# Kernel optimization log

Measured on AMD Instinct MI355X. Metric: run time of the kernel, lower is better.

Reference implementation:

```python
import math
import jax, jax.numpy as jnp
import numpy as np


def setup_inputs() -> dict:
    key = jax.random.key(0)
    k1, k2, k3 = jax.random.split(key, 3)
    B, CK, CV = 2, 64, 384
    T, H, W = 8, 30, 54
    N = T * H * W
    mk = jax.random.normal(k1, (B, CK, N), dtype=jnp.float32)
    qk = jax.random.normal(k2, (B, CK, H, W), dtype=jnp.float32)
    mv = jax.random.normal(k3, (B, CV, N), dtype=jnp.float32)
    return {"mk": mk, "qk": qk, "mv": mv, "topk": 20}


def _compute_affinity(mk, qk, topk):
    # mk: [B, CK, N] memory keys; qk: [B, CK, H, W] query keys
    B, CK, H, W = qk.shape
    M = H * W
    qk2 = qk.reshape(B, CK, M)                      # [B, CK, M]
    a_sq = jnp.sum(mk * mk, axis=1)[:, :, None]     # [B, N, 1]
    ab = jnp.einsum('bcn,bcm->bnm', mk, qk2)        # [B, N, M]
    affinity = (2.0 * ab - a_sq) / math.sqrt(CK)    # negative sq-distance / sqrt(CK)
    N = affinity.shape[1]
    k = min(topk, N)
    # top-k over the memory axis (dim 1): move it last for lax.top_k
    aff_t = jnp.swapaxes(affinity, 1, 2)            # [B, M, N]
    vals, idx = jax.lax.top_k(aff_t, k)             # [B, M, k]
    vals = jax.nn.softmax(vals, axis=-1)
    b_ix = jnp.arange(B)[:, None, None]
    m_ix = jnp.arange(M)[None, :, None]
    sparse = jnp.zeros_like(aff_t).at[b_ix, m_ix, idx].set(vals)  # scatter softmaxed top-k
    return jnp.swapaxes(sparse, 1, 2)               # [B, N, M]


def reference(mk, qk, mv, topk):
    affinity = _compute_affinity(mk, qk, topk)      # [B, N, M]
    mem = jnp.einsum('bcn,bnm->bcm', mv, affinity)  # propagate_feat: bmm(mv, affinity)
    return mem
```

## Files before the change

### kernel.cpp

```cpp
#include <hip/hip_runtime.h>
#include <math.h>
#include <float.h>
#include <limits.h>
#include <stdint.h>

namespace {

constexpr int B  = 2;
constexpr int CK = 64;
constexpr int N  = 12960;
constexpr int M  = 1620;
constexpr int CV = 384;
constexpr int K  = 20;

constexpr int SEGN  = 1024;
constexpr int NSEG  = (N + SEGN - 1) / SEGN;
constexpr int CAP   = 64;
constexpr int SLOTS = NSEG * CAP;
constexpr int JC    = (SLOTS + 255) / 256;

static_assert((CAP & (CAP - 1)) == 0, "CAP must be pow2 (slot>>6 indexing)");
static_assert(NSEG * SEGN >= N, "segments must cover N");

__device__ __forceinline__ uint32_t f2k(float x) {
  uint32_t u = __float_as_uint(x);
  return u ^ ((u & 0x80000000u) ? 0xFFFFFFFFu : 0x80000000u);
}
__device__ __forceinline__ float k2f(uint32_t k) {
  uint32_t u = (k & 0x80000000u) ? (k ^ 0x80000000u) : ~k;
  return __uint_as_float(u);
}

__global__ __launch_bounds__(256) void transpose_kernel(const float* __restrict__ mv,
                                                        float* __restrict__ mvT) {
  __shared__ float tile[64][65];
  int b = blockIdx.z;
  int n0 = blockIdx.x * 64;
  int c0 = blockIdx.y * 64;
  int tx = threadIdx.x & 63, ty = threadIdx.x >> 6;
  for (int r = ty; r < 64; r += 4) {
    int c = c0 + r, n = n0 + tx;
    tile[r][tx] = (n < N) ? mv[((size_t)b * CV + c) * N + n] : 0.f;
  }
  __syncthreads();
  for (int r = ty; r < 64; r += 4) {
    int n = n0 + r, c = c0 + tx;
    if (n < N) mvT[((size_t)b * N + n) * CV + c] = tile[tx][r];
  }
}

__global__ __launch_bounds__(256) void transpose_out_kernel(const float* __restrict__ outT,
                                                            float* __restrict__ out) {
  __shared__ float tile[64][65];
  int b = blockIdx.z;
  int m0 = blockIdx.x * 64;
  int c0 = blockIdx.y * 64;
  int tx = threadIdx.x & 63, ty = threadIdx.x >> 6;
  for (int r = ty; r < 64; r += 4) {
    int m = m0 + r;
    if (m < M) tile[r][tx] = outT[((size_t)b * M + m) * CV + c0 + tx];
  }
  __syncthreads();
  for (int r = ty; r < 64; r += 4) {
    int c = c0 + r, m = m0 + tx;
    if (m < M) out[((size_t)b * CV + c) * M + m] = tile[tx][r];
  }
}

__global__ __launch_bounds__(256) void asq_kernel(const float* __restrict__ mk,
                                                  float* __restrict__ asq) {
  int i = blockIdx.x * 256 + threadIdx.x;
  if (i >= B * N) return;
  int b = i / N, n = i - b * N;
  const float* p = mk + (size_t)b * CK * N + n;
  float s = 0.f;
#pragma unroll
  for (int c = 0; c < CK; ++c) {
    float v = p[(size_t)c * N];
    s += v * v;
  }
  asq[i] = s;
}

template <bool FULL>
__device__ __forceinline__ void emit_round(int r, int b, int seg, int mg0, int l, int w,
                                           uint64_t lmlt,
                                           uint32_t* __restrict__ cnt,
                                           uint2* __restrict__ pairs,
                                           float (&vv)[4][SEGN]) {
  const int m = mg0 + 4 * r + w;
  if (m < M) {
    float vloc[16];
#pragma unroll
    for (int j = 0; j < 4; ++j) {
      const float4 q = *reinterpret_cast<const float4*>(&vv[w][4 * l + 256 * j]);
      vloc[4 * j + 0] = q.x;
      vloc[4 * j + 1] = q.y;
      vloc[4 * j + 2] = q.z;
      vloc[4 * j + 3] = q.w;
    }
    float a0 = fmaxf(fmaxf(vloc[0], vloc[1]), fmaxf(vloc[2], vloc[3]));
    float a1 = fmaxf(fmaxf(vloc[4], vloc[5]), fmaxf(vloc[6], vloc[7]));
    float a2 = fmaxf(fmaxf(vloc[8], vloc[9]), fmaxf(vloc[10], vloc[11]));
    float a3 = fmaxf(fmaxf(vloc[12], vloc[13]), fmaxf(vloc[14], vloc[15]));
    float s = fmaxf(fmaxf(a0, a1), fmaxf(a2, a3));
#pragma unroll
    for (int kk = 2; kk <= 64; kk <<= 1) {
#pragma unroll
      for (int jj = kk >> 1; jj > 0; jj >>= 1) {
        const float o = __shfl_xor(s, jj, 64);
        const bool keepMin = (((l & kk) == 0) == ((l & jj) == 0));
        s = keepMin ? fminf(s, o) : fmaxf(s, o);
      }
    }
    const float th = __shfl(s, 44, 64);
    const size_t pbase = ((size_t)(b * M + m) * NSEG + seg) * CAP;
    int base = 0;
#pragma unroll
    for (int r16 = 0; r16 < 16; ++r16) {
      const bool hit = vloc[r16] >= th;
      const uint64_t mask = __ballot(hit);
      if (hit) {
        const int pos = base + (int)__popcll(mask & lmlt);
        if (pos < CAP)
          pairs[pbase + pos] = make_uint2(
              f2k(vloc[r16]),
              (uint32_t)(seg * SEGN + 4 * l + 256 * (r16 >> 2) + (r16 & 3)));
      }
      base += (int)__popcll(mask);
    }
    if (l == 0)
      cnt[(size_t)(b * M + m) * NSEG + seg] = (uint32_t)(base < CAP ? base : CAP);
  }
}

template <bool FULL>
__device__ __forceinline__ void fused_body(const float* __restrict__ mk,
                                           const float* __restrict__ qk,
                                           const float* __restrict__ asq,
                                           uint32_t* __restrict__ cnt,
                                           uint2* __restrict__ pairs,
                                           float (&qs)[CK][20],
                                           float (&vv)[4][SEGN]) {
  const int b = blockIdx.z;
  const int seg = blockIdx.x;
  const int mg0 = blockIdx.y * 16;
  const int t = threadIdx.x;
  const int l = t & 63, w = t >> 6;

  for (int i = t; i < CK * 16; i += 256) {
    int c = i >> 4, ml = i & 15;
    int m = mg0 + ml;
    qs[c][ml] = (m < M) ? qk[((size_t)b * CK + c) * M + m] : 0.f;
  }
  __syncthreads();

  const int nl0 = w * 256 + 4 * l;
  const int nb  = seg * SEGN + nl0;
  const bool vld = FULL || (nb < N);

  const float* p = mk + (size_t)b * CK * N + nb;

  float4 acc[16];
#pragma unroll
  for (int m = 0; m < 16; ++m) acc[m] = make_float4(0.f, 0.f, 0.f, 0.f);

  auto ld = [&](const float* q) -> float4 {
    return vld ? *reinterpret_cast<const float4*>(q) : make_float4(0.f, 0.f, 0.f, 0.f);
  };
  auto fmastep = [&](const float4& kv, int c) {
    const float4 q0 = *reinterpret_cast<const float4*>(&qs[c][0]);
    const float4 q1 = *reinterpret_cast<const float4*>(&qs[c][4]);
    const float4 q2 = *reinterpret_cast<const float4*>(&qs[c][8]);
    const float4 q3 = *reinterpret_cast<const float4*>(&qs[c][12]);
    const float qm[16] = {q0.x, q0.y, q0.z, q0.w, q1.x, q1.y, q1.z, q1.w,
                          q2.x, q2.y, q2.z, q2.w, q3.x, q3.y, q3.z, q3.w};
#pragma unroll
    for (int m = 0; m < 16; ++m) {
      acc[m].x += kv.x * qm[m];
      acc[m].y += kv.y * qm[m];
      acc[m].z += kv.z * qm[m];
      acc[m].w += kv.w * qm[m];
    }
  };

  float4 kva = ld(p);
  float4 kvb = ld(p + N);
  const float* pn = p + 2 * (size_t)N;
#pragma unroll 2
  for (int c = 0; c < CK - 2; ++c) {
    const float4 kvn = ld(pn);
    pn += N;
    fmastep(kva, c);
    kva = kvb;
    kvb = kvn;
  }
  fmastep(kva, CK - 2);
  fmastep(kvb, CK - 1);

  float4 sq4 = make_float4(0.f, 0.f, 0.f, 0.f);
  if (vld) sq4 = *reinterpret_cast<const float4*>(asq + (size_t)b * N + nb);

  const uint64_t lmlt = (1ull << l) - 1ull;

#pragma unroll
  for (int r = 0; r < 4; ++r) {
#pragma unroll
    for (int mj = 0; mj < 4; ++mj) {
      const float4 a = acc[4 * r + mj];
      float4 vr;
      vr.x = (2.f * a.x - sq4.x) * 0.125f;
      vr.y = (2.f * a.y - sq4.y) * 0.125f;
      vr.z = (2.f * a.z - sq4.z) * 0.125f;
      vr.w = (2.f * a.w - sq4.w) * 0.125f;
      if (!FULL && !vld) vr = make_float4(-FLT_MAX, -FLT_MAX, -FLT_MAX, -FLT_MAX);
      *reinterpret_cast<float4*>(&vv[mj][nl0]) = vr;
    }
    __syncthreads();
    emit_round<FULL>(r, b, seg, mg0, l, w, lmlt, cnt, pairs, vv);
    __syncthreads();
  }
}

__global__ __launch_bounds__(256) void fused_kernel(const float* __restrict__ mk,
                                                    const float* __restrict__ qk,
                                                    const float* __restrict__ asq,
                                                    uint32_t* __restrict__ cnt,
                                                    uint2* __restrict__ pairs) {
  __shared__ float qs[CK][20];
  __shared__ float vv[4][SEGN];
  if (blockIdx.x != NSEG - 1)
    fused_body<true>(mk, qk, asq, cnt, pairs, qs, vv);
  else
    fused_body<false>(mk, qk, asq, cnt, pairs, qs, vv);
}

__global__ __launch_bounds__(256) void merge_topk_gather(const uint32_t* __restrict__ cnt,
                                                         const uint2* __restrict__ pairs,
                                                         const float* __restrict__ mvT,
                                                         float* __restrict__ outT) {
  const int m = blockIdx.x, b = blockIdx.y;
  const int t = threadIdx.x;

  __shared__ uint32_t segc[NSEG];
  constexpr int HP = 268;
  __shared__ int hist[4][4][HP];
  __shared__ int s_digit, s_before;
  __shared__ int wn[K];
  __shared__ uint32_t wk[K];
  __shared__ float sw[K];
  __shared__ int gcnt, ecnt, s_last;
  __shared__ int ebuf[K];
  __shared__ int rmin4[4];

  if (t < NSEG) segc[t] = cnt[(size_t)(b * M + m) * NSEG + t];
  __syncthreads();

  const uint2* pb = pairs + (size_t)(b * M + m) * SLOTS;
  uint32_t k[JC];
  uint32_t nn[JC];
#pragma unroll
  for (int j = 0; j < JC; ++j) {
    int idx = t + (j << 8);
    bool valid = (idx < SLOTS) && ((uint32_t)(idx & (CAP - 1)) < segc[idx >> 6]);
    if (valid) {
      uint2 pr = pb[idx];
      k[j] = pr.x;
      nn[j] = pr.y;
    } else {
      k[j] = 0u;
      nn[j] = 0u;
    }
  }

  int before = 0;
  uint32_t pref = 0;
  const int w = t >> 6;
  const int rp = (t >> 4) & 3;
  int* myhist = &hist[w][rp][0];

  for (int p = 0; p < 4; ++p) {
    const int s = 24 - 8 * p;
    for (int i = t; i < 16 * HP; i += 256) ((int*)hist)[i] = 0;
    __syncthreads();
    const int shHi = (p == 0) ? 0 : (s + 8);
#pragma unroll
    for (int j = 0; j < JC; ++j) {
      uint32_t key = k[j];
      bool act = (p == 0) || ((key >> shHi) == pref);
      if (act) atomicAdd(&myhist[(key >> s) & 255], 1);
    }
    __syncthreads();
    if (t < 64) {
      int d = 4 * t;
      int4 g = make_int4(0, 0, 0, 0);
#pragma unroll
      for (int ww = 0; ww < 4; ++ww)
#pragma unroll
        for (int rr = 0; rr < 4; ++rr) {
          int4 h = *reinterpret_cast<int4*>(&hist[ww][rr][d]);
          g.x += h.x; g.y += h.y; g.z += h.z; g.w += h.w;
        }
      int sl = g.x + g.y + g.z + g.w;
      int sfx = sl;
#pragma unroll
      for (int off = 1; off < 64; off <<= 1) {
        int o = __shfl_down(sfx, off);
        sfx += (t + off < 64) ? o : 0;
      }
      int above = sfx - sl;
      int rem = K - before;
      if (above < rem && rem <= sfx) {
        int cum = above, ds;
        if (cum + g.w >= rem) ds = 3;
        else { cum += g.w;
          if (cum + g.z >= rem) ds = 2;
          else { cum += g.z;
            if (cum + g.y >= rem) ds = 1;
            else { cum += g.y; ds = 0; } } }
        s_digit = 4 * t + ds;
        s_before = before + cum;
      }
    }
    __syncthreads();
    pref = (pref << 8) | (uint32_t)s_digit;
    before = s_before;
  }

  const uint32_t thr = pref;
  const int need = K - before;
  if (t == 0) { gcnt = 0; ecnt = 0; }
  __syncthreads();
#pragma unroll
  for (int j = 0; j < JC; ++j) {
    uint32_t key = k[j];
    if (key > thr) {
      int q = atomicAdd(&gcnt, 1);
      wn[q] = (int)nn[j]; wk[q] = key;
    } else if (key == thr) {
      int q = atomicAdd(&ecnt, 1);
      if (q < K) ebuf[q] = (int)nn[j];
    }
  }
  __syncthreads();
  if (ecnt == need) {
    if (t < need) { wn[before + t] = ebuf[t]; wk[before + t] = thr; }
  } else {
    int last = -1;
    for (int r = 0; r < need; ++r) {
      int loc = INT_MAX;
#pragma unroll
      for (int j = 0; j < JC; ++j) {
        int n = (int)nn[j];
        if (k[j] == thr && n > last && n < loc) loc = n;
      }
#pragma unroll
      for (int off = 1; off < 64; off <<= 1) loc = min(loc, __shfl_xor(loc, off));
      if ((t & 63) == 0) rmin4[t >> 6] = loc;
      __syncthreads();
      if (t == 0) {
        int mn = min(min(rmin4[0], rmin4[1]), min(rmin4[2], rmin4[3]));
        wn[before + r] = mn; wk[before + r] = thr; s_last = mn;
      }
      __syncthreads();
      last = s_last;
    }
  }
  __syncthreads();

  if (t < 64) {
    float v = (t < K) ? k2f(wk[t]) : -FLT_MAX;
    float mx = v;
#pragma unroll
    for (int off = 1; off < 64; off <<= 1) mx = fmaxf(mx, __shfl_xor(mx, off));
    float e = (t < K) ? expf(v - mx) : 0.f;
    float ss = e;
#pragma unroll
    for (int off = 1; off < 64; off <<= 1) ss += __shfl_xor(ss, off);
    if (t < K) sw[t] = e / ss;
  }
  __syncthreads();

  if (t < CV / 4) {
    const float4* tb4 = reinterpret_cast<const float4*>(mvT + (size_t)b * N * CV);
    float4 s4 = make_float4(0.f, 0.f, 0.f, 0.f);
#pragma unroll
    for (int j = 0; j < K; ++j) {
      float wj = sw[j];
      float4 vv4 = tb4[(size_t)wn[j] * (CV / 4) + t];
      s4.x += wj * vv4.x; s4.y += wj * vv4.y; s4.z += wj * vv4.z; s4.w += wj * vv4.w;
    }
    reinterpret_cast<float4*>(outT + ((size_t)b * M + m) * CV)[t] = s4;
  }
}

}

extern "C" void kernel_launch(void* const* d_in, const int* in_sizes, int n_in,
                              void* d_out, int out_size, void* d_ws, size_t ws_size,
                              hipStream_t stream) {
  const float* mk = (const float*)d_in[0];
  const float* qk = (const float*)d_in[1];
  const float* mv = (const float*)d_in[2];
  float* out = (float*)d_out;

  char* w = (char*)d_ws;
  float* asq = (float*)w;
  size_t o = (size_t)B * N * sizeof(float);
  float* mvT = (float*)(w + o);
  o += (size_t)B * N * CV * sizeof(float);
  float* outT = (float*)(w + o);
  o += (size_t)B * M * CV * sizeof(float);
  uint32_t* cnt = (uint32_t*)(w + o);
  o += (size_t)B * M * NSEG * sizeof(uint32_t);
  uint2* pairs = (uint2*)(w + o);
  o += (size_t)B * M * NSEG * CAP * sizeof(uint2);

  transpose_kernel<<<dim3((N + 63) / 64, CV / 64, B), 256, 0, stream>>>(mv, mvT);
  asq_kernel<<<(B * N + 255) / 256, 256, 0, stream>>>(mk, asq);
  const int MG = (M + 15) / 16;
  fused_kernel<<<dim3(NSEG, MG, B), 256, 0, stream>>>(mk, qk, asq, cnt, pairs);
  merge_topk_gather<<<dim3(M, B), 256, 0, stream>>>(cnt, pairs, mvT, outT);
  transpose_out_kernel<<<dim3((M + 63) / 64, CV / 64, B), 256, 0, stream>>>(outT, out);
}
```

Before: 244.4 us.

## Remap fused kernel grid for XCD locality and deepen load prefetch pipeline

The fused distance/candidate kernel now launches on a 1D grid and remaps block IDs so that consecutive logical work-groups (same segment, adjacent m-groups) land on the same XCD. Blocks reading the same mk segment then share that XCD's L2. The inner channel loop also now prefetches four mk rows ahead and double-buffers the qk shared-memory reads in registers. This overlaps global load latency with FMAs, at the cost of more live registers, which could lower occupancy.

```diff
diff --git a/kernel.cpp b/kernel.cpp
--- a/kernel.cpp
+++ b/kernel.cpp
@@ -18,6 +18,7 @@
 constexpr int CAP   = 64;
 constexpr int SLOTS = NSEG * CAP;
 constexpr int JC    = (SLOTS + 255) / 256;
+constexpr int MG    = (M + 15) / 16;
 
 static_assert((CAP & (CAP - 1)) == 0, "CAP must be pow2 (slot>>6 indexing)");
 static_assert(NSEG * SEGN >= N, "segments must cover N");
@@ -140,11 +141,9 @@
                                            const float* __restrict__ asq,
                                            uint32_t* __restrict__ cnt,
                                            uint2* __restrict__ pairs,
+                                           int b, int seg, int mg0,
                                            float (&qs)[CK][20],
                                            float (&vv)[4][SEGN]) {
-  const int b = blockIdx.z;
-  const int seg = blockIdx.x;
-  const int mg0 = blockIdx.y * 16;
   const int t = threadIdx.x;
   const int l = t & 63, w = t >> 6;
 
@@ -165,16 +164,18 @@
 #pragma unroll
   for (int m = 0; m < 16; ++m) acc[m] = make_float4(0.f, 0.f, 0.f, 0.f);
 
-  auto ld = [&](const float* q) -> float4 {
+  auto ldk = [&](const float* q) -> float4 {
     return vld ? *reinterpret_cast<const float4*>(q) : make_float4(0.f, 0.f, 0.f, 0.f);
   };
-  auto fmastep = [&](const float4& kv, int c) {
-    const float4 q0 = *reinterpret_cast<const float4*>(&qs[c][0]);
-    const float4 q1 = *reinterpret_cast<const float4*>(&qs[c][4]);
-    const float4 q2 = *reinterpret_cast<const float4*>(&qs[c][8]);
-    const float4 q3 = *reinterpret_cast<const float4*>(&qs[c][12]);
-    const float qm[16] = {q0.x, q0.y, q0.z, q0.w, q1.x, q1.y, q1.z, q1.w,
-                          q2.x, q2.y, q2.z, q2.w, q3.x, q3.y, q3.z, q3.w};
+  auto ldq = [&](int c, float4 (&q)[4]) {
+    q[0] = *reinterpret_cast<const float4*>(&qs[c][0]);
+    q[1] = *reinterpret_cast<const float4*>(&qs[c][4]);
+    q[2] = *reinterpret_cast<const float4*>(&qs[c][8]);
+    q[3] = *reinterpret_cast<const float4*>(&qs[c][12]);
+  };
+  auto fmastep = [&](const float4& kv, const float4 (&q)[4]) {
+    const float qm[16] = {q[0].x, q[0].y, q[0].z, q[0].w, q[1].x, q[1].y, q[1].z, q[1].w,
+                          q[2].x, q[2].y, q[2].z, q[2].w, q[3].x, q[3].y, q[3].z, q[3].w};
 #pragma unroll
     for (int m = 0; m < 16; ++m) {
       acc[m].x += kv.x * qm[m];
@@ -184,19 +185,40 @@
     }
   };
 
-  float4 kva = ld(p);
-  float4 kvb = ld(p + N);
-  const float* pn = p + 2 * (size_t)N;
-#pragma unroll 2
-  for (int c = 0; c < CK - 2; ++c) {
-    const float4 kvn = ld(pn);
-    pn += N;
-    fmastep(kva, c);
-    kva = kvb;
-    kvb = kvn;
-  }
-  fmastep(kva, CK - 2);
-  fmastep(kvb, CK - 1);
+  float4 kv0 = ldk(p);
+  float4 kv1 = ldk(p + (size_t)N);
+  float4 kv2 = ldk(p + 2 * (size_t)N);
+  float4 kv3 = ldk(p + 3 * (size_t)N);
+  float4 qa[4], qb[4];
+  ldq(0, qa);
+
+  const float* pn = p + 4 * (size_t)N;
+  int c = 0;
+#pragma unroll 1
+  for (int g = 0; g < (CK - 4) / 4; ++g) {
+    float4 n0 = ldk(pn);
+    float4 n1 = ldk(pn + (size_t)N);
+    float4 n2 = ldk(pn + 2 * (size_t)N);
+    float4 n3 = ldk(pn + 3 * (size_t)N);
+    ldq(c + 1, qb);
+    fmastep(kv0, qa);
+    ldq(c + 2, qa);
+    fmastep(kv1, qb);
+    ldq(c + 3, qb);
+    fmastep(kv2, qa);
+    ldq(c + 4, qa);
+    fmastep(kv3, qb);
+    kv0 = n0; kv1 = n1; kv2 = n2; kv3 = n3;
+    pn += 4 * (size_t)N;
+    c += 4;
+  }
+  ldq(61, qb);
+  fmastep(kv0, qa);
+  ldq(62, qa);
+  fmastep(kv1, qb);
+  ldq(63, qb);
+  fmastep(kv2, qa);
+  fmastep(kv3, qb);
 
   float4 sq4 = make_float4(0.f, 0.f, 0.f, 0.f);
   if (vld) sq4 = *reinterpret_cast<const float4*>(asq + (size_t)b * N + nb);
@@ -229,10 +251,22 @@
                                                     uint2* __restrict__ pairs) {
   __shared__ float qs[CK][20];
   __shared__ float vv[4][SEGN];
-  if (blockIdx.x != NSEG - 1)
-    fused_body<true>(mk, qk, asq, cnt, pairs, qs, vv);
+
+  constexpr int NWG = NSEG * MG * B;
+  constexpr int NX = 8;
+  constexpr int Q = NWG / NX, R = NWG % NX;
+  const int orig = blockIdx.x;
+  const int xcd = orig & (NX - 1), idx = orig >> 3;
+  const int wgid = (xcd < R ? xcd * (Q + 1) : R * (Q + 1) + (xcd - R) * Q) + idx;
+  const int segb = wgid / MG;
+  const int mg   = wgid - segb * MG;
+  const int b    = segb / NSEG;
+  const int seg  = segb - b * NSEG;
+
+  if (seg != NSEG - 1)
+    fused_body<true>(mk, qk, asq, cnt, pairs, b, seg, mg * 16, qs, vv);
   else
-    fused_body<false>(mk, qk, asq, cnt, pairs, qs, vv);
+    fused_body<false>(mk, qk, asq, cnt, pairs, b, seg, mg * 16, qs, vv);
 }
 
 __global__ __launch_bounds__(256) void merge_topk_gather(const uint32_t* __restrict__ cnt,
@@ -418,8 +452,7 @@
 
   transpose_kernel<<<dim3((N + 63) / 64, CV / 64, B), 256, 0, stream>>>(mv, mvT);
   asq_kernel<<<(B * N + 255) / 256, 256, 0, stream>>>(mk, asq);
-  const int MG = (M + 15) / 16;
-  fused_kernel<<<dim3(NSEG, MG, B), 256, 0, stream>>>(mk, qk, asq, cnt, pairs);
+  fused_kernel<<<dim3(NSEG * MG * B), 256, 0, stream>>>(mk, qk, asq, cnt, pairs);
   merge_topk_gather<<<dim3(M, B), 256, 0, stream>>>(cnt, pairs, mvT, outT);
   transpose_out_kernel<<<dim3((M + 63) / 64, CV / 64, B), 256, 0, stream>>>(outT, out);
 }
```

Result: slower. 251.9 us (+3.1%).
